# Performance work log

Measured on AMD Instinct MI355X. Metric: run time of the kernel, lower is better.

Reference implementation:

```python
import jax, jax.numpy as jnp
import numpy as np

LOG2 = float(np.log(2.0))

def ssp(v):
    # ShiftedSoftplus: softplus(x) - log(2)
    return jax.nn.softplus(v) - jnp.asarray(LOG2, v.dtype)

def setup_inputs() -> dict:
    key = jax.random.key(0)
    ks = jax.random.split(key, 16)
    N, B, F, R, P = 100000, 128, 64, 32, 1600000
    inp = {
        "x": jax.random.normal(ks[0], (N, B), jnp.float32),
        "f_ij": jax.random.uniform(ks[1], (P, R), jnp.float32),
        "rcut_ij": jax.random.uniform(ks[2], (P,), jnp.float32),
        "pairlist": jax.random.randint(ks[3], (2, P), 0, N, jnp.int64),
        # input_to_feature: Linear(B, F)
        "w_in": jax.random.normal(ks[4], (B, F), jnp.float32) * (1.0 / np.sqrt(B)),
        "b_in": jnp.zeros((F,), jnp.float32),
        # filter_network: Linear(R, F) + SSP, Linear(F, F)
        "w_f1": jax.random.normal(ks[5], (R, F), jnp.float32) * (1.0 / np.sqrt(R)),
        "b_f1": jnp.zeros((F,), jnp.float32),
        "w_f2": jax.random.normal(ks[6], (F, F), jnp.float32) * (1.0 / np.sqrt(F)),
        "b_f2": jnp.zeros((F,), jnp.float32),
        # feature_to_output: Linear(F, B) + SSP, Linear(B, B)
        "w_o1": jax.random.normal(ks[7], (F, B), jnp.float32) * (1.0 / np.sqrt(F)),
        "b_o1": jnp.zeros((B,), jnp.float32),
        "w_o2": jax.random.normal(ks[8], (B, B), jnp.float32) * (1.0 / np.sqrt(B)),
        "b_o2": jnp.zeros((B,), jnp.float32),
    }
    return inp

def reference(x, f_ij, rcut_ij, pairlist, w_in, b_in, w_f1, b_f1, w_f2, b_f2, w_o1, b_o1, w_o2, b_o2):
    n_atoms = x.shape[0]
    # input_to_feature
    h = x @ w_in + b_in                                    # [N, F]
    # filter_network on rbf features, weighted by cutoff
    Wij = ssp(f_ij @ w_f1 + b_f1) @ w_f2 + b_f2            # [P, F]
    Wij = Wij * rcut_ij[:, None]
    idx_i, idx_j = pairlist[0], pairlist[1]
    # gather neighbor features, modulate, scatter-add to center atoms
    x_ij = h[idx_j] * Wij                                  # [P, F]
    agg = jax.ops.segment_sum(x_ij, idx_i, num_segments=n_atoms)  # [N, F]
    # feature_to_output
    out = ssp(agg @ w_o1 + b_o1) @ w_o2 + b_o2             # [N, B]
    return out
```

## Files before the change

kernel.cpp:

```cpp
#include <hip/hip_runtime.h>
#include <hip/hip_bf16.h>
#include <hip/hip_fp16.h>

#define B_ 128
#define F_ 64
#define R_ 32

typedef __attribute__((ext_vector_type(8))) __bf16 bf16x8;
typedef __attribute__((ext_vector_type(4))) float f32x4;

#define LN2F 0.6931471805599453f
#define L2EF 1.4426950408889634f

__device__ __forceinline__ float sspf(float x) {
    float t = fabsf(x) * (-L2EF);
    float e; asm("v_exp_f32 %0, %1" : "=v"(e) : "v"(t));
    float l; asm("v_log_f32 %0, %1" : "=v"(l) : "v"(1.0f + e));
    return fmaxf(x, 0.0f) + fmaf(LN2F, l, -LN2F);
}
__device__ __forceinline__ float bfbits2f(unsigned int us) { return __uint_as_float(us << 16); }
__device__ __forceinline__ unsigned int f2bf(float f) {
    unsigned int u = __float_as_uint(f);
    return (u + 0x7fffu + ((u >> 16) & 1u)) >> 16;
}
__device__ __forceinline__ float h16f(unsigned short s) { return __half2float(__ushort_as_half(s)); }
__device__ __forceinline__ unsigned int pkbf(float a, float b) {
    __hip_bfloat162 h = __float22bfloat162_rn(make_float2(a, b));
    unsigned int r; __builtin_memcpy(&r, &h, 4); return r;
}
__device__ __forceinline__ unsigned int pkh(float a, float b) {
    __half2 h = __float22half2_rn(make_float2(a, b));
    unsigned int r; __builtin_memcpy(&r, &h, 4); return r;
}

__global__ __launch_bounds__(256) void front_kernel(
    const float* __restrict__ w1, const float* __restrict__ w2,
    const float* __restrict__ wo1, const float* __restrict__ wo2,
    unsigned short* __restrict__ w1p, unsigned short* __restrict__ w2p,
    unsigned short* __restrict__ wo1p, unsigned short* __restrict__ wo2p,
    const void* __restrict__ pl, int* __restrict__ flag, int P,
    const float* __restrict__ x, const float* __restrict__ w_in,
    const float* __restrict__ b_in, unsigned short* __restrict__ h, int NA,
    int* __restrict__ hist, int hgrid)
{
    int b = blockIdx.x;
    if (b < 15) {
        int t = b * 256 + threadIdx.x;
        if (t < 256) {
            int ct = t >> 6, l = t & 63, g = l >> 4, m = l & 15;
            #pragma unroll
            for (int i = 0; i < 8; ++i)
                w1p[t * 8 + i] = (unsigned short)f2bf(w1[(g * 8 + i) * F_ + ct * 16 + m]);
        } else if (t < 768) {
            int q = t - 256;
            int kh = q >> 8, ct = (q >> 6) & 3, l = q & 63, g = l >> 4, m = l & 15;
            #pragma unroll
            for (int i = 0; i < 8; ++i)
                w2p[q * 8 + i] = (unsigned short)f2bf(w2[(kh * 32 + g * 8 + i) * F_ + ct * 16 + m]);
        } else if (t < 2816) {
            int q = t - 768;
            int l = q & 63, ct = (q >> 6) & 3, kh = (q >> 8) & 3, ch = q >> 10;
            int g = l >> 4, m = l & 15;
            #pragma unroll
            for (int i = 0; i < 8; ++i)
                wo2p[q * 8 + i] = (unsigned short)f2bf(wo2[(kh * 32 + g * 8 + i) * B_ + ch * 64 + ct * 16 + m]);
        } else if (t < 3840) {
            int q = t - 2816;
            int l = q & 63, ct = (q >> 6) & 3, kh = (q >> 8) & 1, ch = q >> 9;
            int g = l >> 4, m = l & 15;
            #pragma unroll
            for (int i = 0; i < 8; ++i)
                wo1p[q * 8 + i] = (unsigned short)f2bf(wo1[(kh * 32 + g * 8 + i) * B_ + ch * 64 + ct * 16 + m]);
        }
        return;
    }
    if (b == 15) {
        if (threadIdx.x < 64) {
            int n = (P < 64) ? P : 64;
            const long long* p64 = (const long long*)pl;
            bool bad = false;
            if ((int)threadIdx.x < n) {
                long long v = p64[threadIdx.x];
                bad = (v < 0) || (v >= 100000000LL);
            }
            unsigned long long bl = __ballot(bad);
            if (threadIdx.x == 0) *flag = (bl == 0ULL) ? 1 : 0;
        }
        return;
    }
    if (b < 16 + hgrid) {
        int n = (b - 16) * 256 + threadIdx.x;
        if (n >= NA) return;
        float acc[F_];
        #pragma unroll
        for (int f = 0; f < F_; ++f) acc[f] = b_in[f];
        const float4* xrow = (const float4*)(x + (size_t)n * B_);
        #pragma unroll 2
        for (int rb = 0; rb < B_ / 4; ++rb) {
            float4 xv = xrow[rb];
            const float* w0 = w_in + (size_t)(4 * rb) * F_;
            #pragma unroll
            for (int f = 0; f < F_; ++f) acc[f] = fmaf(xv.x, w0[f], acc[f]);
            #pragma unroll
            for (int f = 0; f < F_; ++f) acc[f] = fmaf(xv.y, w0[F_ + f], acc[f]);
            #pragma unroll
            for (int f = 0; f < F_; ++f) acc[f] = fmaf(xv.z, w0[2 * F_ + f], acc[f]);
            #pragma unroll
            for (int f = 0; f < F_; ++f) acc[f] = fmaf(xv.w, w0[3 * F_ + f], acc[f]);
        }
        uint4* hrow = (uint4*)(h + (size_t)n * F_);
        #pragma unroll
        for (int q = 0; q < F_ / 8; ++q) {
            uint4 ob;
            ob.x = pkbf(acc[8 * q + 0], acc[8 * q + 1]);
            ob.y = pkbf(acc[8 * q + 2], acc[8 * q + 3]);
            ob.z = pkbf(acc[8 * q + 4], acc[8 * q + 5]);
            ob.w = pkbf(acc[8 * q + 6], acc[8 * q + 7]);
            hrow[q] = ob;
        }
        return;
    }
    __shared__ int sflag;
    if (threadIdx.x < 64) {
        int n = (P < 64) ? P : 64;
        const long long* p64 = (const long long*)pl;
        bool bad = false;
        if ((int)threadIdx.x < n) {
            long long v = p64[threadIdx.x];
            bad = (v < 0) || (v >= 100000000LL);
        }
        unsigned long long bl = __ballot(bad);
        if (threadIdx.x == 0) sflag = (bl == 0ULL) ? 1 : 0;
    }
    __syncthreads();
    int p = (b - 16 - hgrid) * 256 + threadIdx.x;
    if (p >= P) return;
    int i = sflag ? (int)((const long long*)pl)[p] : ((const int*)pl)[p];
    atomicAdd(&hist[i], 1);
}

__global__ __launch_bounds__(256) void scan1_kernel(
    const int* __restrict__ hist, int* __restrict__ off,
    int* __restrict__ bsum, int NA)
{
    __shared__ int s[256];
    int t = threadIdx.x;
    int idx = blockIdx.x * 2048 + t * 8;
    int v[8];
    int run = 0;
    #pragma unroll
    for (int k = 0; k < 8; ++k) {
        int i = idx + k;
        int c = (i < NA) ? hist[i] : 0;
        v[k] = run; run += c;
    }
    s[t] = run;
    __syncthreads();
    for (int o = 1; o < 256; o <<= 1) {
        int x = (t >= o) ? s[t - o] : 0;
        __syncthreads();
        s[t] += x;
        __syncthreads();
    }
    int base = (t == 0) ? 0 : s[t - 1];
    #pragma unroll
    for (int k = 0; k < 8; ++k) {
        int i = idx + k;
        if (i < NA) off[i] = v[k] + base;
    }
    if (t == 255) bsum[blockIdx.x] = s[255];
}

__global__ __launch_bounds__(256) void scan2_kernel(int* __restrict__ bsum, int nb) {
    __shared__ int s[256];
    int t = threadIdx.x;
    int v = (t < nb) ? bsum[t] : 0;
    s[t] = v;
    __syncthreads();
    for (int o = 1; o < 256; o <<= 1) {
        int x = (t >= o) ? s[t - o] : 0;
        __syncthreads();
        s[t] += x;
        __syncthreads();
    }
    if (t < nb) bsum[t] = s[t] - v;
}

__global__ __launch_bounds__(256) void scan3_kernel(
    int* __restrict__ off, int* __restrict__ cursor,
    const int* __restrict__ bsum, int NA, int P)
{
    int i = blockIdx.x * 256 + threadIdx.x;
    if (i > NA) return;
    if (i == NA) { off[NA] = P; return; }
    int v = off[i] + bsum[i >> 11];
    off[i] = v;
    cursor[i] = v;
}

template <bool ATOMIC>
__global__ __launch_bounds__(256, 4) void pair_kernel(
    const float* __restrict__ f_ij, const float* __restrict__ rcut,
    const void* __restrict__ pl, const int* __restrict__ flag,
    const unsigned short* __restrict__ w1p, const float* __restrict__ b1,
    const unsigned short* __restrict__ w2p, const float* __restrict__ b2,
    const unsigned short* __restrict__ h, unsigned short* __restrict__ xs,
    int* __restrict__ cursor, float* __restrict__ agg_f32, int P)
{
    __shared__ __align__(16) unsigned short T[256 * 64];
    __shared__ __align__(16) int   ii[256];
    __shared__ __align__(16) int   jj[256];
    __shared__ __align__(16) float rr[256];

    const int tid   = threadIdx.x;
    const int lane  = tid & 63;
    const int wv    = tid >> 6;
    const int g     = lane >> 4;
    const int m     = lane & 15;
    const int pbase = blockIdx.x * 256;
    const int wbase = wv * 64;

    {
        int p = pbase + tid;
        bool valid = (p < P);
        int pc = valid ? p : (P > 0 ? P - 1 : 0);
        long long i_, j_;
        if (*flag) {
            const long long* p64 = (const long long*)pl;
            i_ = p64[pc]; j_ = p64[(size_t)P + pc];
        } else {
            const int* p32 = (const int*)pl;
            i_ = p32[pc]; j_ = p32[(size_t)P + pc];
        }
        jj[tid] = valid ? (int)j_ : 0;
        rr[tid] = valid ? rcut[pc] : 0.0f;
        if (ATOMIC) {
            ii[tid] = valid ? (int)i_ : 0;
        } else {
            ii[tid] = valid ? atomicAdd(&cursor[(int)i_], 1) : (P + tid);
        }
    }

    bf16x8 w1f[4], w2f[2][4];
    #pragma unroll
    for (int ct = 0; ct < 4; ++ct)
        w1f[ct] = *(const bf16x8*)&w1p[(ct * 64 + lane) * 8];
    #pragma unroll
    for (int kh = 0; kh < 2; ++kh)
        #pragma unroll
        for (int ct = 0; ct < 4; ++ct)
            w2f[kh][ct] = *(const bf16x8*)&w2p[((kh * 4 + ct) * 64 + lane) * 8];

    float4 b1v[4], b2v[4];
    #pragma unroll
    for (int ft = 0; ft < 4; ++ft) {
        b1v[ft] = *(const float4*)&b1[ft * 16 + g * 4];
        b2v[ft] = *(const float4*)&b2[ft * 16 + g * 4];
    }

    bf16x8 fijf[4];
    #pragma unroll
    for (int pt = 0; pt < 4; ++pt) {
        int row = pbase + wbase + pt * 16 + m;
        if (row >= P) row = (P > 0 ? P - 1 : 0);
        const float* srcp = f_ij + (size_t)row * R_ + g * 8;
        float4 f0 = *(const float4*)srcp;
        float4 f1 = *(const float4*)(srcp + 4);
        uint4 pk;
        pk.x = pkbf(f0.x, f0.y);
        pk.y = pkbf(f0.z, f0.w);
        pk.z = pkbf(f1.x, f1.y);
        pk.w = pkbf(f1.z, f1.w);
        bf16x8 av; __builtin_memcpy(&av, &pk, 16);
        fijf[pt] = av;
    }
    f32x4 C1[4][4];
    #pragma unroll
    for (int ft = 0; ft < 4; ++ft)
        #pragma unroll
        for (int pt = 0; pt < 4; ++pt) {
            f32x4 z = {0.f, 0.f, 0.f, 0.f};
            C1[ft][pt] = __builtin_amdgcn_mfma_f32_16x16x32_bf16(w1f[ft], fijf[pt], z, 0, 0, 0);
        }

    #pragma unroll
    for (int ft = 0; ft < 4; ++ft)
        #pragma unroll
        for (int pt = 0; pt < 4; ++pt) {
            int wp = pt * 16 + m;
            float v0 = sspf(C1[ft][pt][0] + b1v[ft].x);
            float v1 = sspf(C1[ft][pt][1] + b1v[ft].y);
            float v2 = sspf(C1[ft][pt][2] + b1v[ft].z);
            float v3 = sspf(C1[ft][pt][3] + b1v[ft].w);
            uint2 tw;
            tw.x = pkbf(v0, v1);
            tw.y = pkbf(v2, v3);
            int c = (ft * 4 + g) ^ ((wp & 7) << 1);
            *(uint2*)&T[(wbase + wp) * 64 + c * 4] = tw;
        }

    ushort4 hcur[4], hnxt[4];
    {
        int j_ = jj[wbase + m];
        const unsigned short* hrow = h + (size_t)j_ * F_;
        #pragma unroll
        for (int ft = 0; ft < 4; ++ft)
            hcur[ft] = *(const ushort4*)&hrow[ft * 16 + g * 4];
    }
    #pragma unroll
    for (int pt = 0; pt < 4; ++pt) {
        if (pt < 3) {
            int j_ = jj[wbase + (pt + 1) * 16 + m];
            const unsigned short* hrow = h + (size_t)j_ * F_;
            #pragma unroll
            for (int ft = 0; ft < 4; ++ft)
                hnxt[ft] = *(const ushort4*)&hrow[ft * 16 + g * 4];
        }

        int wpr = pt * 16 + m;
        int s = wpr & 7;
        const unsigned short* Trow = &T[(wbase + wpr) * 64];
        bf16x8 t0 = *(const bf16x8*)&Trow[((0 + g) ^ s) * 8];
        bf16x8 t1 = *(const bf16x8*)&Trow[((4 + g) ^ s) * 8];
        f32x4 C2f[4];
        #pragma unroll
        for (int ft = 0; ft < 4; ++ft) {
            f32x4 c = {0.f, 0.f, 0.f, 0.f};
            c = __builtin_amdgcn_mfma_f32_16x16x32_bf16(w2f[0][ft], t0, c, 0, 0, 0);
            c = __builtin_amdgcn_mfma_f32_16x16x32_bf16(w2f[1][ft], t1, c, 0, 0, 0);
            C2f[ft] = c;
        }

        int pp = wbase + pt * 16 + m;
        float rc = rr[pp];
        if (!ATOMIC) {
            unsigned short* xrow = xs + (size_t)ii[pp] * F_;
            #pragma unroll
            for (int ft = 0; ft < 4; ++ft) {
                int f0 = ft * 16 + g * 4;
                ushort4 hv = hcur[ft];
                float x0 = (C2f[ft][0] + b2v[ft].x) * rc * bfbits2f(hv.x);
                float x1 = (C2f[ft][1] + b2v[ft].y) * rc * bfbits2f(hv.y);
                float x2 = (C2f[ft][2] + b2v[ft].z) * rc * bfbits2f(hv.z);
                float x3 = (C2f[ft][3] + b2v[ft].w) * rc * bfbits2f(hv.w);
                uint2 w;
                w.x = pkh(x0, x1);
                w.y = pkh(x2, x3);
                *(uint2*)&xrow[f0] = w;
            }
        } else {
            float* aggrow = agg_f32 + (size_t)ii[pp] * F_;
            #pragma unroll
            for (int ft = 0; ft < 4; ++ft) {
                int f0 = ft * 16 + g * 4;
                ushort4 hv = hcur[ft];
                atomicAdd(aggrow + f0 + 0, (C2f[ft][0] + b2v[ft].x) * rc * bfbits2f(hv.x));
                atomicAdd(aggrow + f0 + 1, (C2f[ft][1] + b2v[ft].y) * rc * bfbits2f(hv.y));
                atomicAdd(aggrow + f0 + 2, (C2f[ft][2] + b2v[ft].z) * rc * bfbits2f(hv.z));
                atomicAdd(aggrow + f0 + 3, (C2f[ft][3] + b2v[ft].w) * rc * bfbits2f(hv.w));
            }
        }
        #pragma unroll
        for (int ft = 0; ft < 4; ++ft) hcur[ft] = hnxt[ft];
    }
}

__global__ __launch_bounds__(256) void reduce_kernel(
    const unsigned short* __restrict__ xs, const int* __restrict__ off,
    unsigned short* __restrict__ aggb, int NA)
{
    int a = blockIdx.x * 4 + (threadIdx.x >> 6);
    int lane = threadIdx.x & 63;
    if (a >= NA) return;
    int s = off[a], e = off[a + 1];
    float a0 = 0.f, a1 = 0.f, a2 = 0.f, a3 = 0.f;
    int k = s;
    for (; k + 4 <= e; k += 4) {
        a0 += h16f(xs[(size_t)(k + 0) * F_ + lane]);
        a1 += h16f(xs[(size_t)(k + 1) * F_ + lane]);
        a2 += h16f(xs[(size_t)(k + 2) * F_ + lane]);
        a3 += h16f(xs[(size_t)(k + 3) * F_ + lane]);
    }
    for (; k < e; ++k) a0 += h16f(xs[(size_t)k * F_ + lane]);
    aggb[(size_t)a * F_ + lane] = (unsigned short)f2bf((a0 + a1) + (a2 + a3));
}

template <bool AGGB>
__global__ __launch_bounds__(256) void out12_kernel(
    const void* __restrict__ agg_p,
    const unsigned short* __restrict__ wo1p, const float* __restrict__ b_o1,
    const unsigned short* __restrict__ wo2p, const float* __restrict__ b_o2,
    float* __restrict__ out, int NA)
{
    __shared__ __align__(16) unsigned short U[4][64][136];

    const int tid  = threadIdx.x;
    const int lane = tid & 63;
    const int wv   = tid >> 6;
    const int g    = lane >> 4;
    const int m    = lane & 15;
    const int rbase = blockIdx.x * 256 + wv * 64;

    {
        bf16x8 wf[2][2][4];
        #pragma unroll
        for (int ch = 0; ch < 2; ++ch)
            #pragma unroll
            for (int kh = 0; kh < 2; ++kh)
                #pragma unroll
                for (int ct = 0; ct < 4; ++ct)
                    wf[ch][kh][ct] = *(const bf16x8*)&wo1p[(((ch * 2 + kh) * 4 + ct) * 64 + lane) * 8];
        float4 bo1[2][4];
        #pragma unroll
        for (int ch = 0; ch < 2; ++ch)
            #pragma unroll
            for (int ct = 0; ct < 4; ++ct)
                bo1[ch][ct] = *(const float4*)&b_o1[ch * 64 + ct * 16 + g * 4];

        #pragma unroll
        for (int rt = 0; rt < 4; ++rt) {
            int row = rbase + rt * 16 + m;
            if (row >= NA) row = NA - 1;
            bf16x8 af[2];
            #pragma unroll
            for (int kh = 0; kh < 2; ++kh) {
                if (AGGB) {
                    af[kh] = *(const bf16x8*)((const unsigned short*)agg_p + (size_t)row * F_ + kh * 32 + g * 8);
                } else {
                    const float* ar = (const float*)agg_p + (size_t)row * F_ + kh * 32 + g * 8;
                    float4 v0 = *(const float4*)ar;
                    float4 v1 = *(const float4*)(ar + 4);
                    uint4 pk;
                    pk.x = pkbf(v0.x, v0.y); pk.y = pkbf(v0.z, v0.w);
                    pk.z = pkbf(v1.x, v1.y); pk.w = pkbf(v1.z, v1.w);
                    bf16x8 av; __builtin_memcpy(&av, &pk, 16);
                    af[kh] = av;
                }
            }
            #pragma unroll
            for (int ch = 0; ch < 2; ++ch)
                #pragma unroll
                for (int ct = 0; ct < 4; ++ct) {
                    f32x4 c = {0.f, 0.f, 0.f, 0.f};
                    c = __builtin_amdgcn_mfma_f32_16x16x32_bf16(wf[ch][0][ct], af[0], c, 0, 0, 0);
                    c = __builtin_amdgcn_mfma_f32_16x16x32_bf16(wf[ch][1][ct], af[1], c, 0, 0, 0);
                    float u0 = sspf(c[0] + bo1[ch][ct].x);
                    float u1 = sspf(c[1] + bo1[ch][ct].y);
                    float u2 = sspf(c[2] + bo1[ch][ct].z);
                    float u3 = sspf(c[3] + bo1[ch][ct].w);
                    uint2 uw;
                    uw.x = pkbf(u0, u1);
                    uw.y = pkbf(u2, u3);
                    *(uint2*)&U[wv][rt * 16 + m][ch * 64 + ct * 16 + g * 4] = uw;
                }
        }
    }

    #pragma unroll
    for (int ch = 0; ch < 2; ++ch) {
        bf16x8 wf2[4][4];
        #pragma unroll
        for (int kh = 0; kh < 4; ++kh)
            #pragma unroll
            for (int ct = 0; ct < 4; ++ct)
                wf2[kh][ct] = *(const bf16x8*)&wo2p[(((ch * 4 + kh) * 4 + ct) * 64 + lane) * 8];
        float bo2[4];
        #pragma unroll
        for (int ct = 0; ct < 4; ++ct) bo2[ct] = b_o2[ch * 64 + ct * 16 + m];

        #pragma unroll
        for (int rt = 0; rt < 4; ++rt) {
            bf16x8 af[4];
            #pragma unroll
            for (int kh = 0; kh < 4; ++kh)
                af[kh] = *(const bf16x8*)&U[wv][rt * 16 + m][kh * 32 + g * 8];
            #pragma unroll
            for (int ct = 0; ct < 4; ++ct) {
                f32x4 c = {0.f, 0.f, 0.f, 0.f};
                #pragma unroll
                for (int kh = 0; kh < 4; ++kh)
                    c = __builtin_amdgcn_mfma_f32_16x16x32_bf16(af[kh], wf2[kh][ct], c, 0, 0, 0);
                #pragma unroll
                for (int r = 0; r < 4; ++r) {
                    int ro = rbase + rt * 16 + g * 4 + r;
                    if (ro < NA)
                        out[(size_t)ro * B_ + ch * 64 + ct * 16 + m] = c[r] + bo2[ct];
                }
            }
        }
    }
}

extern "C" void kernel_launch(void* const* d_in, const int* in_sizes, int n_in,
                              void* d_out, int out_size, void* d_ws, size_t ws_size,
                              hipStream_t stream) {
    const float* x    = (const float*)d_in[0];
    const float* f_ij = (const float*)d_in[1];
    const float* rcut = (const float*)d_in[2];
    const void*  pl   = d_in[3];
    const float* w_in = (const float*)d_in[4];
    const float* b_in = (const float*)d_in[5];
    const float* w_f1 = (const float*)d_in[6];
    const float* b_f1 = (const float*)d_in[7];
    const float* w_f2 = (const float*)d_in[8];
    const float* b_f2 = (const float*)d_in[9];
    const float* w_o1 = (const float*)d_in[10];
    const float* b_o1 = (const float*)d_in[11];
    const float* w_o2 = (const float*)d_in[12];
    const float* b_o2 = (const float*)d_in[13];
    float* out = (float*)d_out;

    int NA = in_sizes[0] / B_;
    int P  = in_sizes[2];
    int nb = (NA + 2047) / 2048;
    int hgrid = (NA + 255) / 256;
    int pgrid = (P + 255) / 256;

    size_t hB    = (size_t)NA * F_ * 2;
    size_t xsB   = (size_t)(P + 256) * F_ * 2;
    size_t agB   = (size_t)NA * F_ * 2;
    size_t histB = (size_t)NA * 4;
    size_t offB  = (size_t)(NA + 1) * 4;
    size_t curB  = (size_t)NA * 4;
    size_t wAll  = (2048 + 4096 + 8192 + 16384) * 2;
    size_t mainNeed = hB + xsB + agB + histB + offB + curB + 1024 + wAll + 8192;

    bool CSR = (ws_size >= mainNeed) && (nb <= 256);

    char* ws = (char*)d_ws;
    size_t off_ = 0;
    auto alloc = [&](size_t bytes) { size_t o = off_; off_ = (off_ + bytes + 255) & ~(size_t)255; return o; };

    unsigned short* h_buf = (unsigned short*)(ws + alloc(hB));
    unsigned short* w1p   = (unsigned short*)(ws + alloc(2048 * 2));
    unsigned short* w2p   = (unsigned short*)(ws + alloc(4096 * 2));
    unsigned short* wo1p  = (unsigned short*)(ws + alloc(8192 * 2));
    unsigned short* wo2p  = (unsigned short*)(ws + alloc(16384 * 2));
    int* flag             = (int*)(ws + alloc(256));

    if (CSR) {
        unsigned short* xs   = (unsigned short*)(ws + alloc(xsB));
        unsigned short* aggb = (unsigned short*)(ws + alloc(agB));
        int* hist            = (int*)(ws + alloc(histB));
        int* off             = (int*)(ws + alloc(offB));
        int* cursor          = (int*)(ws + alloc(curB));
        int* bsum            = (int*)(ws + alloc(1024));

        (void)hipMemsetAsync(hist, 0, histB, stream);
        front_kernel<<<16 + hgrid + pgrid, 256, 0, stream>>>(
            w_f1, w_f2, w_o1, w_o2, w1p, w2p, wo1p, wo2p,
            pl, flag, P, x, w_in, b_in, h_buf, NA, hist, hgrid);
        scan1_kernel<<<nb, 256, 0, stream>>>(hist, off, bsum, NA);
        scan2_kernel<<<1, 256, 0, stream>>>(bsum, nb);
        scan3_kernel<<<(NA + 1 + 255) / 256, 256, 0, stream>>>(off, cursor, bsum, NA, P);
        pair_kernel<false><<<pgrid, 256, 0, stream>>>(
            f_ij, rcut, pl, flag, w1p, b_f1, w2p, b_f2, h_buf, xs, cursor, nullptr, P);
        reduce_kernel<<<(NA + 3) / 4, 256, 0, stream>>>(xs, off, aggb, NA);
        out12_kernel<true><<<hgrid, 256, 0, stream>>>(aggb, wo1p, b_o1, wo2p, b_o2, out, NA);
    } else {
        float* agg = (float*)(ws + alloc((size_t)NA * F_ * 4));
        (void)hipMemsetAsync(agg, 0, (size_t)NA * F_ * 4, stream);
        front_kernel<<<16 + hgrid, 256, 0, stream>>>(
            w_f1, w_f2, w_o1, w_o2, w1p, w2p, wo1p, wo2p,
            pl, flag, P, x, w_in, b_in, h_buf, NA, nullptr, hgrid);
        pair_kernel<true><<<pgrid, 256, 0, stream>>>(
            f_ij, rcut, pl, flag, w1p, b_f1, w2p, b_f2, h_buf, nullptr, nullptr, agg, P);
        out12_kernel<false><<<hgrid, 256, 0, stream>>>(agg, wo1p, b_o1, wo2p, b_o2, out, NA);
    }
}
```

Measured before the change: 383.3 us.

## Move neighbor feature gather from pair kernel into CSR reduce kernel

The pair kernel no longer gathers h[j] per pair. It writes the filter weights (times cutoff) to the sorted slot and records j in a new jslot array. The reduce kernel then gathers h[j] via jslot and does a multiply-accumulate while summing each atom's segment. This removes the random h gather and its prefetch registers from the heavy pair kernel, but adds a 4-byte-per-pair jslot write and read, plus dependent indirect loads in the reduce loop.

```diff
diff --git a/kernel.cpp b/kernel.cpp
--- a/kernel.cpp
+++ b/kernel.cpp
@@ -205,7 +205,8 @@
     const unsigned short* __restrict__ w1p, const float* __restrict__ b1,
     const unsigned short* __restrict__ w2p, const float* __restrict__ b2,
     const unsigned short* __restrict__ h, unsigned short* __restrict__ xs,
-    int* __restrict__ cursor, float* __restrict__ agg_f32, int P)
+    int* __restrict__ cursor, int* __restrict__ jslot,
+    float* __restrict__ agg_f32, int P)
 {
     __shared__ __align__(16) unsigned short T[256 * 64];
     __shared__ __align__(16) int   ii[256];
@@ -237,7 +238,9 @@
         if (ATOMIC) {
             ii[tid] = valid ? (int)i_ : 0;
         } else {
-            ii[tid] = valid ? atomicAdd(&cursor[(int)i_], 1) : (P + tid);
+            int pos = valid ? atomicAdd(&cursor[(int)i_], 1) : (P + tid);
+            ii[tid] = pos;
+            if (valid) jslot[pos] = (int)j_;
         }
     }
 
@@ -299,24 +302,8 @@
             *(uint2*)&T[(wbase + wp) * 64 + c * 4] = tw;
         }
 
-    ushort4 hcur[4], hnxt[4];
-    {
-        int j_ = jj[wbase + m];
-        const unsigned short* hrow = h + (size_t)j_ * F_;
-        #pragma unroll
-        for (int ft = 0; ft < 4; ++ft)
-            hcur[ft] = *(const ushort4*)&hrow[ft * 16 + g * 4];
-    }
     #pragma unroll
     for (int pt = 0; pt < 4; ++pt) {
-        if (pt < 3) {
-            int j_ = jj[wbase + (pt + 1) * 16 + m];
-            const unsigned short* hrow = h + (size_t)j_ * F_;
-            #pragma unroll
-            for (int ft = 0; ft < 4; ++ft)
-                hnxt[ft] = *(const ushort4*)&hrow[ft * 16 + g * 4];
-        }
-
         int wpr = pt * 16 + m;
         int s = wpr & 7;
         const unsigned short* Trow = &T[(wbase + wpr) * 64];
@@ -338,35 +325,35 @@
             #pragma unroll
             for (int ft = 0; ft < 4; ++ft) {
                 int f0 = ft * 16 + g * 4;
-                ushort4 hv = hcur[ft];
-                float x0 = (C2f[ft][0] + b2v[ft].x) * rc * bfbits2f(hv.x);
-                float x1 = (C2f[ft][1] + b2v[ft].y) * rc * bfbits2f(hv.y);
-                float x2 = (C2f[ft][2] + b2v[ft].z) * rc * bfbits2f(hv.z);
-                float x3 = (C2f[ft][3] + b2v[ft].w) * rc * bfbits2f(hv.w);
+                float x0 = (C2f[ft][0] + b2v[ft].x) * rc;
+                float x1 = (C2f[ft][1] + b2v[ft].y) * rc;
+                float x2 = (C2f[ft][2] + b2v[ft].z) * rc;
+                float x3 = (C2f[ft][3] + b2v[ft].w) * rc;
                 uint2 w;
                 w.x = pkh(x0, x1);
                 w.y = pkh(x2, x3);
                 *(uint2*)&xrow[f0] = w;
             }
         } else {
+            int j_ = jj[pp];
+            const unsigned short* hrow = h + (size_t)j_ * F_;
             float* aggrow = agg_f32 + (size_t)ii[pp] * F_;
             #pragma unroll
             for (int ft = 0; ft < 4; ++ft) {
                 int f0 = ft * 16 + g * 4;
-                ushort4 hv = hcur[ft];
+                ushort4 hv = *(const ushort4*)&hrow[f0];
                 atomicAdd(aggrow + f0 + 0, (C2f[ft][0] + b2v[ft].x) * rc * bfbits2f(hv.x));
                 atomicAdd(aggrow + f0 + 1, (C2f[ft][1] + b2v[ft].y) * rc * bfbits2f(hv.y));
                 atomicAdd(aggrow + f0 + 2, (C2f[ft][2] + b2v[ft].z) * rc * bfbits2f(hv.z));
                 atomicAdd(aggrow + f0 + 3, (C2f[ft][3] + b2v[ft].w) * rc * bfbits2f(hv.w));
             }
         }
-        #pragma unroll
-        for (int ft = 0; ft < 4; ++ft) hcur[ft] = hnxt[ft];
     }
 }
 
 __global__ __launch_bounds__(256) void reduce_kernel(
-    const unsigned short* __restrict__ xs, const int* __restrict__ off,
+    const unsigned short* __restrict__ xs, const int* __restrict__ jslot,
+    const int* __restrict__ off, const unsigned short* __restrict__ h,
     unsigned short* __restrict__ aggb, int NA)
 {
     int a = blockIdx.x * 4 + (threadIdx.x >> 6);
@@ -376,12 +363,26 @@
     float a0 = 0.f, a1 = 0.f, a2 = 0.f, a3 = 0.f;
     int k = s;
     for (; k + 4 <= e; k += 4) {
-        a0 += h16f(xs[(size_t)(k + 0) * F_ + lane]);
-        a1 += h16f(xs[(size_t)(k + 1) * F_ + lane]);
-        a2 += h16f(xs[(size_t)(k + 2) * F_ + lane]);
-        a3 += h16f(xs[(size_t)(k + 3) * F_ + lane]);
-    }
-    for (; k < e; ++k) a0 += h16f(xs[(size_t)k * F_ + lane]);
+        int j0 = jslot[k + 0], j1 = jslot[k + 1];
+        int j2 = jslot[k + 2], j3 = jslot[k + 3];
+        float w0 = h16f(xs[(size_t)(k + 0) * F_ + lane]);
+        float w1 = h16f(xs[(size_t)(k + 1) * F_ + lane]);
+        float w2 = h16f(xs[(size_t)(k + 2) * F_ + lane]);
+        float w3 = h16f(xs[(size_t)(k + 3) * F_ + lane]);
+        float h0 = bfbits2f(h[(size_t)j0 * F_ + lane]);
+        float h1 = bfbits2f(h[(size_t)j1 * F_ + lane]);
+        float h2 = bfbits2f(h[(size_t)j2 * F_ + lane]);
+        float h3 = bfbits2f(h[(size_t)j3 * F_ + lane]);
+        a0 = fmaf(w0, h0, a0);
+        a1 = fmaf(w1, h1, a1);
+        a2 = fmaf(w2, h2, a2);
+        a3 = fmaf(w3, h3, a3);
+    }
+    for (; k < e; ++k) {
+        int j0 = jslot[k];
+        a0 = fmaf(h16f(xs[(size_t)k * F_ + lane]),
+                  bfbits2f(h[(size_t)j0 * F_ + lane]), a0);
+    }
     aggb[(size_t)a * F_ + lane] = (unsigned short)f2bf((a0 + a1) + (a2 + a3));
 }
 
@@ -522,8 +523,9 @@
     size_t histB = (size_t)NA * 4;
     size_t offB  = (size_t)(NA + 1) * 4;
     size_t curB  = (size_t)NA * 4;
+    size_t jsB   = (size_t)(P + 256) * 4;
     size_t wAll  = (2048 + 4096 + 8192 + 16384) * 2;
-    size_t mainNeed = hB + xsB + agB + histB + offB + curB + 1024 + wAll + 8192;
+    size_t mainNeed = hB + xsB + agB + histB + offB + curB + jsB + 1024 + wAll + 8192;
 
     bool CSR = (ws_size >= mainNeed) && (nb <= 256);
 
@@ -544,6 +546,7 @@
         int* hist            = (int*)(ws + alloc(histB));
         int* off             = (int*)(ws + alloc(offB));
         int* cursor          = (int*)(ws + alloc(curB));
+        int* jslot           = (int*)(ws + alloc(jsB));
         int* bsum            = (int*)(ws + alloc(1024));
 
         (void)hipMemsetAsync(hist, 0, histB, stream);
@@ -554,8 +557,8 @@
         scan2_kernel<<<1, 256, 0, stream>>>(bsum, nb);
         scan3_kernel<<<(NA + 1 + 255) / 256, 256, 0, stream>>>(off, cursor, bsum, NA, P);
         pair_kernel<false><<<pgrid, 256, 0, stream>>>(
-            f_ij, rcut, pl, flag, w1p, b_f1, w2p, b_f2, h_buf, xs, cursor, nullptr, P);
-        reduce_kernel<<<(NA + 3) / 4, 256, 0, stream>>>(xs, off, aggb, NA);
+            f_ij, rcut, pl, flag, w1p, b_f1, w2p, b_f2, h_buf, xs, cursor, jslot, nullptr, P);
+        reduce_kernel<<<(NA + 3) / 4, 256, 0, stream>>>(xs, jslot, off, h_buf, aggb, NA);
         out12_kernel<true><<<hgrid, 256, 0, stream>>>(aggb, wo1p, b_o1, wo2p, b_o2, out, NA);
     } else {
         float* agg = (float*)(ws + alloc((size_t)NA * F_ * 4));
@@ -564,7 +567,7 @@
             w_f1, w_f2, w_o1, w_o2, w1p, w2p, wo1p, wo2p,
             pl, flag, P, x, w_in, b_in, h_buf, NA, nullptr, hgrid);
         pair_kernel<true><<<pgrid, 256, 0, stream>>>(
-            f_ij, rcut, pl, flag, w1p, b_f1, w2p, b_f2, h_buf, nullptr, nullptr, agg, P);
+            f_ij, rcut, pl, flag, w1p, b_f1, w2p, b_f2, h_buf, nullptr, nullptr, nullptr, agg, P);
         out12_kernel<false><<<hgrid, 256, 0, stream>>>(agg, wo1p, b_o1, wo2p, b_o2, out, NA);
     }
 }
```

Measured after the change: 409.9 us. +7.0%, slower.
